# Kernel tuning notes

Hardware: AMD Instinct MI355X
Metric: run time of the kernel (lower is better)

Reference implementation:

```python
import jax, jax.numpy as jnp
import numpy as np

B, R, H = 64, 32, 1024  # batch, num_rounds, lstm_hidden_size
IN = 2 * H              # GatedTrans in_dim
EPS = 1e-12             # F.normalize eps


def _gated(x, Wy, by, Wg, bg):
    # GatedTrans: tanh branch * leaky_relu branch (slope 0.01, torch default)
    return jnp.tanh(x @ Wy + by) * jax.nn.leaky_relu(x @ Wg + bg, 0.01)


def setup_inputs() -> dict:
    key = jax.random.key(0)
    ks = jax.random.split(key, 12)
    s_in = 1.0 / np.sqrt(IN)
    s_h = 1.0 / np.sqrt(H)
    return {
        "hist": jax.random.normal(ks[0], (B, R, IN), jnp.float32),
        "ques": jax.random.normal(ks[1], (B, R, IN), jnp.float32),
        "W_hy": jax.random.normal(ks[2], (IN, H), jnp.float32) * s_in,
        "b_hy": jnp.zeros((H,), jnp.float32),
        "W_hg": jax.random.normal(ks[3], (IN, H), jnp.float32) * s_in,
        "b_hg": jnp.zeros((H,), jnp.float32),
        "W_qy": jax.random.normal(ks[4], (IN, H), jnp.float32) * s_in,
        "b_qy": jnp.zeros((H,), jnp.float32),
        "W_qg": jax.random.normal(ks[5], (IN, H), jnp.float32) * s_in,
        "b_qg": jnp.zeros((H,), jnp.float32),
        "W_att": jax.random.normal(ks[6], (H,), jnp.float32) * s_h,
        "b_att": jnp.zeros((), jnp.float32),
    }


def reference(hist, ques, W_hy, b_hy, W_hg, b_hg, W_qy, b_qy, W_qg, b_qg, W_att, b_att):
    hist_embed = _gated(hist, W_hy, b_hy, W_hg, b_hg)   # [B, R, H]
    ques_embed = _gated(ques, W_qy, b_qy, W_qg, b_qg)   # [B, R, H]
    # broadcast outer product over rounds: [B, Rq, Rh, H]
    att_embed = ques_embed[:, :, None, :] * hist_embed[:, None, :, :]
    norm = jnp.sqrt(jnp.sum(att_embed * att_embed, axis=-1, keepdims=True))
    att_embed = att_embed / jnp.maximum(norm, EPS)       # F.normalize(p=2)
    scores = att_embed @ W_att + b_att                   # [B, Rq, Rh]
    att = jax.nn.softmax(scores, axis=-1)
    tril = jnp.tril(jnp.ones((R, R), jnp.float32))       # causal round mask
    att_masked = att * tril
    att_masked = att_masked / jnp.sum(att_masked, axis=-1, keepdims=True)
    # weighted sum over hist rounds: [B, Rq, 2H]
    feat = jnp.einsum("bqh,bhd->bqd", att_masked, hist)
    return feat
```

## Files before the change

kernel.cpp:

```cpp
#include <hip/hip_runtime.h>
#include <cstdint>

#define IN_DIM 2048
#define H_DIM  1024
#define BROWS  2048
#define BATCH  64
#define ROUNDS 32

typedef __bf16 bf16x8 __attribute__((ext_vector_type(8)));
typedef float  f32x4  __attribute__((ext_vector_type(4)));
typedef unsigned short u16;

__device__ __forceinline__ u16 f2bf(float f) {
    unsigned int u = __float_as_uint(f);
    u += 0x7FFFu + ((u >> 16) & 1u);
    return (u16)(u >> 16);
}

__device__ __forceinline__ void async_ld16(const void* g, void* l) {
    __builtin_amdgcn_global_load_lds(
        (__attribute__((address_space(1))) void*)(uintptr_t)g,
        (__attribute__((address_space(3))) void*)(unsigned int)(uintptr_t)l,
        16, 0, 0);
}

__global__ __launch_bounds__(256) void prep(
    const float* __restrict__ hist, const float* __restrict__ ques,
    u16* __restrict__ xh, u16* __restrict__ xq,
    const float* __restrict__ why, const float* __restrict__ whg,
    const float* __restrict__ wqy, const float* __restrict__ wqg,
    u16* __restrict__ oh, u16* __restrict__ oq)
{
    int idx = blockIdx.x;
    if (idx < 4096) {
        int i = idx * 256 + threadIdx.x;
        const float4* h4 = (const float4*)hist;
        const float4* q4 = (const float4*)ques;
        float4 a = h4[i], b = q4[i];
        ushort4 oa, ob;
        oa.x = f2bf(a.x); oa.y = f2bf(a.y); oa.z = f2bf(a.z); oa.w = f2bf(a.w);
        ob.x = f2bf(b.x); ob.y = f2bf(b.y); ob.z = f2bf(b.z); ob.w = f2bf(b.w);
        ((ushort4*)xh)[i] = oa;
        ((ushort4*)xq)[i] = ob;
        return;
    }
    __shared__ float t[32][33];
    int zz = idx - 4096;
    int z = zz >> 12, rem = zz & 4095;
    const float* Y = z == 0 ? why : wqy;
    const float* G = z == 0 ? whg : wqg;
    u16* O = z == 0 ? oh : oq;
    int n0 = (rem & 63) * 32, k0 = (rem >> 6) * 32;
    int tx = threadIdx.x & 31, ty = threadIdx.x >> 5;
    const float* S = (tx < 16) ? Y : G;
    int sc = (n0 >> 1) + (tx & 15);
    #pragma unroll
    for (int r = 0; r < 4; r++)
        t[ty + 8*r][tx] = S[(size_t)(k0 + ty + 8*r) * H_DIM + sc];
    __syncthreads();
    #pragma unroll
    for (int r = 0; r < 4; r++)
        O[(size_t)(n0 + ty + 8*r) * IN_DIM + k0 + tx] = f2bf(t[tx][ty + 8*r]);
}

__global__ __launch_bounds__(256) void gemm_act(
    const u16* __restrict__ xh, const u16* __restrict__ xq,
    const u16* __restrict__ wth, const u16* __restrict__ wtq,
    const float* __restrict__ bhy, const float* __restrict__ bhg,
    const float* __restrict__ bqy, const float* __restrict__ bqg,
    u16* __restrict__ eh, u16* __restrict__ eq)
{
    int L = blockIdx.x;
    int cluster = L & 7;
    int slot = L >> 3;
    int z  = cluster >> 2;
    int y  = (cluster & 1) * 8 + (slot >> 3);
    int x  = ((cluster >> 1) & 1) * 8 + (slot & 7);
    int m0 = y * 128, n0 = x * 128;

    const u16* A  = z == 0 ? xh : xq;
    const u16* Bt = z == 0 ? wth : wtq;
    const float* by = z == 0 ? bhy : bqy;
    const float* bg = z == 0 ? bhg : bqg;
    u16* E = z == 0 ? eh : eq;

    __shared__ __align__(16) u16 As[2][128 * 64];
    __shared__ __align__(16) u16 Bs[2][128 * 64];

    int tid = threadIdx.x;
    int wave = tid >> 6, lane = tid & 63;
    int lane15 = lane & 15, quad = lane >> 4;
    int wm = (wave >> 1) * 64, wn = (wave & 1) * 64;

    f32x4 acc[4][4];
    #pragma unroll
    for (int i = 0; i < 4; i++)
        #pragma unroll
        for (int j = 0; j < 4; j++) acc[i][j] = (f32x4){0.f, 0.f, 0.f, 0.f};

    int srow[4], skc[4], scb[4];
    #pragma unroll
    for (int r2 = 0; r2 < 4; r2++) {
        int cbase = r2 * 256 + wave * 64;
        int cs = cbase + lane;
        int row = cs >> 3, s = cs & 7;
        srow[r2] = row; skc[r2] = s ^ (row & 7); scb[r2] = cbase;
    }

    #define STAGE(buf, kt)                                                                   \
        _Pragma("unroll")                                                                    \
        for (int r2 = 0; r2 < 4; r2++) {                                                     \
            async_ld16(A  + (size_t)(m0 + srow[r2]) * IN_DIM + (kt) + skc[r2] * 8,           \
                       &As[buf][scb[r2] * 8]);                                               \
            async_ld16(Bt + (size_t)(n0 + srow[r2]) * IN_DIM + (kt) + skc[r2] * 8,           \
                       &Bs[buf][scb[r2] * 8]);                                               \
        }

    #define COMPUTE(buf)                                                                     \
        _Pragma("unroll")                                                                    \
        for (int ks = 0; ks < 2; ks++) {                                                     \
            bf16x8 af[4], bfv[4];                                                            \
            _Pragma("unroll")                                                                \
            for (int i = 0; i < 4; i++) {                                                    \
                int row = wm + i * 16 + lane15;                                              \
                int s = (ks * 4 + quad) ^ (row & 7);                                         \
                af[i] = *(const bf16x8*)&As[buf][row * 64 + s * 8];                          \
            }                                                                                \
            _Pragma("unroll")                                                                \
            for (int j = 0; j < 4; j++) {                                                    \
                int row = wn + j * 16 + lane15;                                              \
                int s = (ks * 4 + quad) ^ (row & 7);                                         \
                bfv[j] = *(const bf16x8*)&Bs[buf][row * 64 + s * 8];                         \
            }                                                                                \
            _Pragma("unroll")                                                                \
            for (int i = 0; i < 4; i++)                                                      \
                _Pragma("unroll")                                                            \
                for (int j = 0; j < 4; j++)                                                  \
                    acc[i][j] = __builtin_amdgcn_mfma_f32_16x16x32_bf16(                     \
                        af[i], bfv[j], acc[i][j], 0, 0, 0);                                  \
        }

    STAGE(0, 0)
    for (int kt = 0; kt < IN_DIM; kt += 128) {
        __syncthreads();
        STAGE(1, kt + 64)
        COMPUTE(0)
        __syncthreads();
        if (kt + 128 < IN_DIM) STAGE(0, kt + 128)
        COMPUTE(1)
    }
    #undef STAGE
    #undef COMPUTE

    int n0w = n0 + wn;
    #pragma unroll
    for (int jp = 0; jp < 2; jp++) {
        int hc = (n0w >> 1) + jp * 16 + lane15;
        float vy = by[hc], vg = bg[hc];
        #pragma unroll
        for (int i = 0; i < 4; i++) {
            #pragma unroll
            for (int r = 0; r < 4; r++) {
                int row = m0 + wm + i * 16 + quad * 4 + r;
                float y2 = tanhf(acc[i][2 * jp][r] + vy);
                float g = acc[i][2 * jp + 1][r] + vg;
                E[(size_t)row * H_DIM + hc] = f2bf(y2 * (g > 0.f ? g : 0.01f * g));
            }
        }
    }
}

__global__ __launch_bounds__(256) void score_feat(
    const u16* __restrict__ eh, const u16* __restrict__ eq,
    const float* __restrict__ hist, const float* __restrict__ watt,
    const float* __restrict__ batt, float* __restrict__ out)
{
    int idx = blockIdx.x;
    int b = idx & 63, q = idx >> 6;
    int tid = threadIdx.x, wave = tid >> 6, lane = tid & 63;
    __shared__ float sw[32], swn[32];

    const u16* qe = eq + (size_t)(b * ROUNDS + q) * H_DIM;
    float uw[16], u2[16];
    #pragma unroll
    for (int c = 0; c < 2; c++) {
        uint4 pk = ((const uint4*)qe)[lane + 64 * c];
        float4 w0 = ((const float4*)watt)[(lane + 64 * c) * 2];
        float4 w1 = ((const float4*)watt)[(lane + 64 * c) * 2 + 1];
        unsigned int ws[4] = {pk.x, pk.y, pk.z, pk.w};
        float wf[8] = {w0.x, w0.y, w0.z, w0.w, w1.x, w1.y, w1.z, w1.w};
        #pragma unroll
        for (int e = 0; e < 4; e++) {
            float lo = __uint_as_float(ws[e] << 16);
            float hi = __uint_as_float(ws[e] & 0xFFFF0000u);
            uw[c * 8 + 2 * e]     = lo * wf[2 * e];
            u2[c * 8 + 2 * e]     = lo * lo;
            uw[c * 8 + 2 * e + 1] = hi * wf[2 * e + 1];
            u2[c * 8 + 2 * e + 1] = hi * hi;
        }
    }
    for (int h = wave; h <= q; h += 4) {
        const u16* he = eh + (size_t)(b * ROUNDS + h) * H_DIM;
        float num = 0.f, nrm = 0.f;
        #pragma unroll
        for (int c = 0; c < 2; c++) {
            uint4 pk = ((const uint4*)he)[lane + 64 * c];
            unsigned int vs[4] = {pk.x, pk.y, pk.z, pk.w};
            #pragma unroll
            for (int e = 0; e < 4; e++) {
                float lo = __uint_as_float(vs[e] << 16);
                float hi = __uint_as_float(vs[e] & 0xFFFF0000u);
                num += uw[c * 8 + 2 * e] * lo + uw[c * 8 + 2 * e + 1] * hi;
                nrm += u2[c * 8 + 2 * e] * lo * lo + u2[c * 8 + 2 * e + 1] * hi * hi;
            }
        }
        #pragma unroll
        for (int off = 32; off > 0; off >>= 1) {
            num += __shfl_down(num, off);
            nrm += __shfl_down(nrm, off);
        }
        if (lane == 0)
            sw[h] = num / fmaxf(sqrtf(nrm), 1e-12f) + batt[0];
    }
    __syncthreads();
    if (tid == 0) {
        float mx = -1e30f;
        for (int h = 0; h <= q; h++) mx = fmaxf(mx, sw[h]);
        float zs = 0.f;
        for (int h = 0; h <= q; h++) { float e = expf(sw[h] - mx); swn[h] = e; zs += e; }
        float inv = 1.f / zs;
        for (int h = 0; h <= q; h++) swn[h] *= inv;
    }
    __syncthreads();
    const float4* hb = (const float4*)(hist + (size_t)b * ROUNDS * IN_DIM);
    float4* ob = (float4*)(out + (size_t)(b * ROUNDS + q) * IN_DIM);
    #pragma unroll
    for (int d0 = 0; d0 < 2; d0++) {
        int d = tid + d0 * 256;
        float4 a = {0.f, 0.f, 0.f, 0.f};
        for (int h = 0; h <= q; h++) {
            float w = swn[h];
            float4 x = hb[h * 512 + d];
            a.x += w * x.x; a.y += w * x.y; a.z += w * x.z; a.w += w * x.w;
        }
        ob[d] = a;
    }
}

extern "C" void kernel_launch(void* const* d_in, const int* in_sizes, int n_in,
                              void* d_out, int out_size, void* d_ws, size_t ws_size,
                              hipStream_t stream) {
    const float* hist = (const float*)d_in[0];
    const float* ques = (const float*)d_in[1];
    const float* Why  = (const float*)d_in[2];
    const float* bhy  = (const float*)d_in[3];
    const float* Whg  = (const float*)d_in[4];
    const float* bhg  = (const float*)d_in[5];
    const float* Wqy  = (const float*)d_in[6];
    const float* bqy  = (const float*)d_in[7];
    const float* Wqg  = (const float*)d_in[8];
    const float* bqg  = (const float*)d_in[9];
    const float* watt = (const float*)d_in[10];
    const float* batt = (const float*)d_in[11];
    float* out = (float*)d_out;

    char* w = (char*)d_ws;
    u16* Xh  = (u16*)w;
    u16* Xq  = Xh  + (size_t)BROWS * IN_DIM;
    u16* WtH = Xq  + (size_t)BROWS * IN_DIM;
    u16* WtQ = WtH + (size_t)IN_DIM * IN_DIM;
    u16* Eh  = WtQ + (size_t)IN_DIM * IN_DIM;
    u16* Eq  = Eh  + (size_t)BROWS * H_DIM;

    prep<<<12288, 256, 0, stream>>>(hist, ques, Xh, Xq, Why, Whg, Wqy, Wqg, WtH, WtQ);
    gemm_act<<<512, 256, 0, stream>>>(Xh, Xq, WtH, WtQ, bhy, bhg, bqy, bqg, Eh, Eq);
    score_feat<<<2048, 256, 0, stream>>>(Eh, Eq, hist, watt, batt, out);
}
```

Before: 188.6 us.

## Enlarge GEMM tile to 256x128 with 512 threads and explicit waitcnt pipelining

The gated GEMM kernel now uses 256x128 output tiles computed by 8 waves per block, launching 256 blocks instead of 512. The K loop is rewritten with explicit s_waitcnt/s_barrier control: fragments are read into registers before the next stage's async loads are issued, and the MFMA block runs under raised wave priority. The aim is more reuse of each B tile and better overlap of global-to-LDS loads with matrix math. In exchange the block uses more LDS, and the hand-written wait counts tie correctness to the exact number of outstanding loads.

```diff
diff --git a/kernel.cpp b/kernel.cpp
--- a/kernel.cpp
+++ b/kernel.cpp
@@ -23,6 +23,11 @@
         (__attribute__((address_space(3))) void*)(unsigned int)(uintptr_t)l,
         16, 0, 0);
 }
+
+#define BAR()    asm volatile("s_barrier" ::: "memory")
+#define LGKM0()  asm volatile("s_waitcnt lgkmcnt(0)" ::: "memory")
+#define VMCNT6() asm volatile("s_waitcnt vmcnt(6)" ::: "memory")
+#define VMCNT0() asm volatile("s_waitcnt vmcnt(0)" ::: "memory")
 
 __global__ __launch_bounds__(256) void prep(
     const float* __restrict__ hist, const float* __restrict__ ques,
@@ -63,7 +68,7 @@
         O[(size_t)(n0 + ty + 8*r) * IN_DIM + k0 + tx] = f2bf(t[tx][ty + 8*r]);
 }
 
-__global__ __launch_bounds__(256) void gemm_act(
+__global__ __launch_bounds__(512, 2) void gemm_act(
     const u16* __restrict__ xh, const u16* __restrict__ xq,
     const u16* __restrict__ wth, const u16* __restrict__ wtq,
     const float* __restrict__ bhy, const float* __restrict__ bhg,
@@ -73,10 +78,10 @@
     int L = blockIdx.x;
     int cluster = L & 7;
     int slot = L >> 3;
-    int z  = cluster >> 2;
-    int y  = (cluster & 1) * 8 + (slot >> 3);
-    int x  = ((cluster >> 1) & 1) * 8 + (slot & 7);
-    int m0 = y * 128, n0 = x * 128;
+    int z = cluster >> 2;
+    int y = (cluster & 1) * 4 + (slot >> 3);
+    int x = ((cluster >> 1) & 1) * 8 + (slot & 7);
+    int m0 = y * 256, n0 = x * 128;
 
     const u16* A  = z == 0 ? xh : xq;
     const u16* Bt = z == 0 ? wth : wtq;
@@ -84,13 +89,14 @@
     const float* bg = z == 0 ? bhg : bqg;
     u16* E = z == 0 ? eh : eq;
 
-    __shared__ __align__(16) u16 As[2][128 * 64];
+    __shared__ __align__(16) u16 As[2][256 * 64];
     __shared__ __align__(16) u16 Bs[2][128 * 64];
 
     int tid = threadIdx.x;
     int wave = tid >> 6, lane = tid & 63;
     int lane15 = lane & 15, quad = lane >> 4;
-    int wm = (wave >> 1) * 64, wn = (wave & 1) * 64;
+    int wm = (wave & 3) * 64;
+    int wn = (wave >> 2) * 64;
 
     f32x4 acc[4][4];
     #pragma unroll
@@ -98,59 +104,83 @@
         #pragma unroll
         for (int j = 0; j < 4; j++) acc[i][j] = (f32x4){0.f, 0.f, 0.f, 0.f};
 
-    int srow[4], skc[4], scb[4];
+    int sArow[4], sAkc[4], sAcb[4];
     #pragma unroll
     for (int r2 = 0; r2 < 4; r2++) {
-        int cbase = r2 * 256 + wave * 64;
+        int cbase = r2 * 512 + wave * 64;
         int cs = cbase + lane;
         int row = cs >> 3, s = cs & 7;
-        srow[r2] = row; skc[r2] = s ^ (row & 7); scb[r2] = cbase;
-    }
-
-    #define STAGE(buf, kt)                                                                   \
-        _Pragma("unroll")                                                                    \
-        for (int r2 = 0; r2 < 4; r2++) {                                                     \
-            async_ld16(A  + (size_t)(m0 + srow[r2]) * IN_DIM + (kt) + skc[r2] * 8,           \
-                       &As[buf][scb[r2] * 8]);                                               \
-            async_ld16(Bt + (size_t)(n0 + srow[r2]) * IN_DIM + (kt) + skc[r2] * 8,           \
-                       &Bs[buf][scb[r2] * 8]);                                               \
-        }
-
-    #define COMPUTE(buf)                                                                     \
-        _Pragma("unroll")                                                                    \
-        for (int ks = 0; ks < 2; ks++) {                                                     \
-            bf16x8 af[4], bfv[4];                                                            \
-            _Pragma("unroll")                                                                \
-            for (int i = 0; i < 4; i++) {                                                    \
-                int row = wm + i * 16 + lane15;                                              \
-                int s = (ks * 4 + quad) ^ (row & 7);                                         \
-                af[i] = *(const bf16x8*)&As[buf][row * 64 + s * 8];                          \
-            }                                                                                \
-            _Pragma("unroll")                                                                \
-            for (int j = 0; j < 4; j++) {                                                    \
-                int row = wn + j * 16 + lane15;                                              \
-                int s = (ks * 4 + quad) ^ (row & 7);                                         \
-                bfv[j] = *(const bf16x8*)&Bs[buf][row * 64 + s * 8];                         \
-            }                                                                                \
-            _Pragma("unroll")                                                                \
-            for (int i = 0; i < 4; i++)                                                      \
-                _Pragma("unroll")                                                            \
-                for (int j = 0; j < 4; j++)                                                  \
-                    acc[i][j] = __builtin_amdgcn_mfma_f32_16x16x32_bf16(                     \
-                        af[i], bfv[j], acc[i][j], 0, 0, 0);                                  \
-        }
+        sArow[r2] = row; sAkc[r2] = s ^ (row & 7); sAcb[r2] = cbase;
+    }
+    int sBrow[2], sBkc[2], sBcb[2];
+    #pragma unroll
+    for (int r2 = 0; r2 < 2; r2++) {
+        int cbase = r2 * 512 + wave * 64;
+        int cs = cbase + lane;
+        int row = cs >> 3, s = cs & 7;
+        sBrow[r2] = row; sBkc[r2] = s ^ (row & 7); sBcb[r2] = cbase;
+    }
+
+    #define STAGE(buf, kt)                                                                    \
+        _Pragma("unroll")                                                                     \
+        for (int r2 = 0; r2 < 4; r2++)                                                        \
+            async_ld16(A + (size_t)(m0 + sArow[r2]) * IN_DIM + (kt) + sAkc[r2] * 8,           \
+                       &As[buf][sAcb[r2] * 8]);                                               \
+        _Pragma("unroll")                                                                     \
+        for (int r2 = 0; r2 < 2; r2++)                                                        \
+            async_ld16(Bt + (size_t)(n0 + sBrow[r2]) * IN_DIM + (kt) + sBkc[r2] * 8,          \
+                       &Bs[buf][sBcb[r2] * 8]);
+
+    bf16x8 af[2][4], bfv[2][4];
+
+    #define READF(buf)                                                                        \
+        _Pragma("unroll")                                                                     \
+        for (int ks = 0; ks < 2; ks++) {                                                      \
+            _Pragma("unroll")                                                                 \
+            for (int i = 0; i < 4; i++) {                                                     \
+                int row = wm + i * 16 + lane15;                                               \
+                int s = (ks * 4 + quad) ^ (row & 7);                                          \
+                af[ks][i] = *(const bf16x8*)&As[buf][row * 64 + s * 8];                       \
+                int rowb = wn + i * 16 + lane15;                                              \
+                int sb = (ks * 4 + quad) ^ (rowb & 7);                                        \
+                bfv[ks][i] = *(const bf16x8*)&Bs[buf][rowb * 64 + sb * 8];                    \
+            }                                                                                 \
+        }
+
+    #define DOMFMA()                                                                          \
+        __builtin_amdgcn_s_setprio(1);                                                        \
+        _Pragma("unroll")                                                                     \
+        for (int ks = 0; ks < 2; ks++)                                                        \
+            _Pragma("unroll")                                                                 \
+            for (int i = 0; i < 4; i++)                                                       \
+                _Pragma("unroll")                                                             \
+                for (int j = 0; j < 4; j++)                                                   \
+                    acc[i][j] = __builtin_amdgcn_mfma_f32_16x16x32_bf16(                      \
+                        af[ks][i], bfv[ks][j], acc[i][j], 0, 0, 0);                           \
+        __builtin_amdgcn_s_setprio(0);
 
     STAGE(0, 0)
+    STAGE(1, 64)
+    VMCNT6(); BAR();
+
+    #pragma unroll 1
     for (int kt = 0; kt < IN_DIM; kt += 128) {
-        __syncthreads();
-        STAGE(1, kt + 64)
-        COMPUTE(0)
-        __syncthreads();
-        if (kt + 128 < IN_DIM) STAGE(0, kt + 128)
-        COMPUTE(1)
+        READF(0)
+        if (kt + 128 < IN_DIM) { LGKM0(); BAR(); STAGE(0, kt + 128) }
+        DOMFMA()
+        if (kt + 128 < IN_DIM) { VMCNT6(); } else { VMCNT0(); }
+        BAR();
+        READF(1)
+        if (kt + 192 < IN_DIM) { LGKM0(); BAR(); STAGE(1, kt + 192) }
+        DOMFMA()
+        if (kt + 128 < IN_DIM) {
+            if (kt + 192 < IN_DIM) { VMCNT6(); } else { VMCNT0(); }
+            BAR();
+        }
     }
     #undef STAGE
-    #undef COMPUTE
+    #undef READF
+    #undef DOMFMA
 
     int n0w = n0 + wn;
     #pragma unroll
@@ -273,6 +303,6 @@
     u16* Eq  = Eh  + (size_t)BROWS * H_DIM;
 
     prep<<<12288, 256, 0, stream>>>(hist, ques, Xh, Xq, Why, Whg, Wqy, Wqg, WtH, WtQ);
-    gemm_act<<<512, 256, 0, stream>>>(Xh, Xq, WtH, WtQ, bhy, bhg, bqy, bqg, Eh, Eq);
+    gemm_act<<<256, 512, 0, stream>>>(Xh, Xq, WtH, WtQ, bhy, bhg, bqy, bqg, Eh, Eq);
     score_feat<<<2048, 256, 0, stream>>>(Eh, Eq, hist, watt, batt, out);
 }
```

Result: faster. 183.0 us (-2.9%).
